# Kernel tuning notes

Measured on AMD Instinct MI355X. Metric: run time of the kernel, lower is better.

Reference implementation:

```python
import jax, jax.numpy as jnp
import numpy as np

NB_HEAD = 16
SIZE_PER_HEAD = 64
D_MODEL = NB_HEAD * SIZE_PER_HEAD  # 1024
B, L = 2, 2048
NEG_BIG = 1e12


def setup_inputs() -> dict:
    key = jax.random.key(0)
    ks = jax.random.split(key, 8)
    return {
        "Q_seq": jax.random.normal(ks[0], (B, L, D_MODEL), dtype=jnp.float32),
        "K_seq": jax.random.normal(ks[1], (B, L, D_MODEL), dtype=jnp.float32),
        "V_seq": jax.random.normal(ks[2], (B, L, D_MODEL), dtype=jnp.float32),
        "q_len": jax.random.randint(ks[3], (B, 1), 1, L, dtype=jnp.int32),
        "v_len": jax.random.randint(ks[4], (B, 1), 1, L, dtype=jnp.int32),
        "WQ": jax.random.normal(ks[5], (D_MODEL, D_MODEL), dtype=jnp.float32) * 0.02,
        "WK": jax.random.normal(ks[6], (D_MODEL, D_MODEL), dtype=jnp.float32) * 0.02,
        "WV": jax.random.normal(ks[7], (D_MODEL, D_MODEL), dtype=jnp.float32) * 0.02,
    }


def _len_mask(lens, length, dtype):
    # Keras code: mask = 1 - cumsum(one_hot(len, L)) -> 1 for pos < len, 0 otherwise
    return (jnp.arange(length)[None, :] < lens).astype(dtype)  # [B, L]


def reference(Q_seq, K_seq, V_seq, q_len, v_len, WQ, WK, WV):
    Bq, Lq, _ = Q_seq.shape
    Lk = K_seq.shape[1]
    # QKV projections, split heads: [B, H, L, D]
    q = (Q_seq @ WQ).reshape(Bq, Lq, NB_HEAD, SIZE_PER_HEAD).transpose(0, 2, 1, 3)
    k = (K_seq @ WK).reshape(Bq, Lk, NB_HEAD, SIZE_PER_HEAD).transpose(0, 2, 1, 3)
    v = (V_seq @ WV).reshape(Bq, Lk, NB_HEAD, SIZE_PER_HEAD).transpose(0, 2, 1, 3)
    # scaled dot-product scores [B, H, Lq, Lk]
    scores = jnp.einsum("bhqd,bhkd->bhqk", q, k) / np.float32(SIZE_PER_HEAD ** 0.5)
    # additive key-length mask (V_len), matching Mask(..., 'add')
    kmask = _len_mask(v_len, Lk, scores.dtype)  # [B, Lk]
    scores = scores - (1.0 - kmask)[:, None, None, :] * np.float32(NEG_BIG)
    A = jax.nn.softmax(scores, axis=-1)
    # attention output, merge heads: [B, Lq, H*D]
    O = jnp.einsum("bhqk,bhkd->bqhd", A, v).reshape(Bq, Lq, D_MODEL)
    # multiplicative query-length mask (Q_len), matching Mask(..., 'mul')
    qmask = _len_mask(q_len, Lq, O.dtype)  # [B, Lq]
    return O * qmask[:, :, None]
```

## Files before the change

kernel.cpp:

```cpp
#include <hip/hip_runtime.h>
#include <cstddef>

#define NB_HEAD 16
#define HEAD_DIM 64
#define D_MODEL 1024
#define BATCH 2
#define SEQ 2048
#define MROWS (BATCH * SEQ)
#define NSPLIT 2

typedef __bf16 bf16x8 __attribute__((ext_vector_type(8)));
typedef __bf16 bf16x4 __attribute__((ext_vector_type(4)));
typedef float  f32x4  __attribute__((ext_vector_type(4)));

#define XEL ((size_t)MROWS * D_MODEL)
#define WEL ((size_t)D_MODEL * D_MODEL)

#define QSCALE 0.18033688011112042f

static __device__ __forceinline__ size_t xchunk(int row, int k) {
    return ((size_t)(row >> 4) * 32 + (k >> 5)) * 512 + ((k >> 3) & 3) * 128 + (row & 15) * 8 + (k & 7);
}
static __device__ __forceinline__ size_t qkbase(int bh, int row16, int dc) {
    return ((size_t)(bh * 128 + row16) * 2 + dc) * 512;
}
static __device__ __forceinline__ size_t qkelem(int bh, int row, int d) {
    return qkbase(bh, row >> 4, d >> 5) + ((d >> 3) & 3) * 128 + (row & 15) * 8 + (d & 7);
}
static __device__ __forceinline__ size_t vbase(int bh, int d16, int kc) {
    return ((size_t)(bh * 4 + d16) * 64 + kc) * 512;
}
static __device__ __forceinline__ size_t velem(int bh, int d, int key) {
    return vbase(bh, d >> 4, key >> 5) + ((key >> 3) & 3) * 128 + (d & 15) * 8 + (key & 7);
}

static __device__ __forceinline__ void split_bf16(float x, __bf16& h, __bf16& l) {
    h = (__bf16)x;
    l = (__bf16)(x - (float)h);
}

static __device__ __forceinline__ void gload_lds16(const __bf16* g, __bf16* l) {
    __builtin_amdgcn_global_load_lds((const __attribute__((address_space(1))) void*)g,
                                     (__attribute__((address_space(3))) void*)l,
                                     16, 0, 0);
}

__global__ __launch_bounds__(256) void conv_wt_kernel(
    const float* __restrict__ W0, const float* __restrict__ W1,
    const float* __restrict__ W2,
    __bf16* __restrict__ hi, __bf16* __restrict__ lo)
{
    __shared__ float tile[64][65];
    const int t  = threadIdx.x;
    const int k0 = blockIdx.x * 64;
    const int n0 = blockIdx.y * 64;
    const int z  = blockIdx.z;
    const float* W = (z == 0) ? W0 : ((z == 1) ? W1 : W2);
    __bf16* hz = hi + (size_t)z * WEL;
    __bf16* lz = lo + (size_t)z * WEL;

    #pragma unroll
    for (int p = 0; p < 4; ++p) {
        const int e = (p * 256 + t) * 4;
        const int r = e >> 6, c = e & 63;
        const float4 v = *(const float4*)(W + (size_t)(k0 + r) * D_MODEL + n0 + c);
        tile[r][c] = v.x; tile[r][c + 1] = v.y; tile[r][c + 2] = v.z; tile[r][c + 3] = v.w;
    }
    __syncthreads();
    #pragma unroll
    for (int p = 0; p < 4; ++p) {
        const int e = (p * 256 + t) * 4;
        const int n = e >> 6, kc = e & 63;
        __bf16 h[4], l[4];
        #pragma unroll
        for (int u = 0; u < 4; ++u) split_bf16(tile[kc + u][n], h[u], l[u]);
        const size_t a = xchunk(n0 + n, k0 + kc);
        *(bf16x4*)(hz + a) = (bf16x4){h[0], h[1], h[2], h[3]};
        *(bf16x4*)(lz + a) = (bf16x4){l[0], l[1], l[2], l[3]};
    }
}

__global__ __launch_bounds__(256) void conv_x_kernel(
    const float* __restrict__ X0, const float* __restrict__ X1,
    const float* __restrict__ X2,
    const int* __restrict__ q_len, const int* __restrict__ v_len,
    __bf16* __restrict__ xhi, __bf16* __restrict__ xlo)
{
    const int z = blockIdx.y;
    const size_t e = ((size_t)blockIdx.x * 256 + threadIdx.x) * 8;
    const int l = (int)(e >> 10), k = (int)(e & 1023);
    const int bb = l >> 11, lb = l & (SEQ - 1);
    const int len = (z == 0) ? q_len[bb] : v_len[bb];
    if (lb >= ((len + 127) & ~127)) return;

    const float* X = (z == 0) ? X0 : ((z == 1) ? X1 : X2);
    const float4 v0 = *(const float4*)(X + e);
    const float4 v1 = *(const float4*)(X + e + 4);
    const float xs[8] = {v0.x, v0.y, v0.z, v0.w, v1.x, v1.y, v1.z, v1.w};
    bf16x8 h8, l8;
    #pragma unroll
    for (int u = 0; u < 8; ++u) { __bf16 h_, l_; split_bf16(xs[u], h_, l_); h8[u] = h_; l8[u] = l_; }
    const size_t a = z * XEL + xchunk(l, k);
    *(bf16x8*)(xhi + a) = h8;
    *(bf16x8*)(xlo + a) = l8;
}

__global__ __launch_bounds__(256, 3) void proj_mfma_kernel(
    const __bf16* __restrict__ Xhi, const __bf16* __restrict__ Xlo,
    const __bf16* __restrict__ Wchi, const __bf16* __restrict__ Wclo,
    const int* __restrict__ q_len, const int* __restrict__ v_len,
    __bf16* __restrict__ qch, __bf16* __restrict__ qcl,
    __bf16* __restrict__ kch, __bf16* __restrict__ kcl,
    __bf16* __restrict__ vch, __bf16* __restrict__ vcl)
{
    __shared__ __align__(16) __bf16 lds[2][24][512];

    const int t    = threadIdx.x;
    const int wave = t >> 6, lane = t & 63;
    const int li   = lane & 15, grp = lane >> 4;
    const int wm   = wave >> 1, wn = wave & 1;
    const int m0   = blockIdx.x * 128;
    const int n0   = blockIdx.y * 64;
    const int z    = blockIdx.z;
    const int bb   = m0 >> 11;
    const int l0   = m0 & (SEQ - 1);
    const int need = (z == 0) ? q_len[bb] : v_len[bb];
    if (l0 >= need) return;

    const __bf16* Xh = Xhi + z * XEL;
    const __bf16* Xl = Xlo + z * XEL;
    const __bf16* Wh = Wchi + z * WEL;
    const __bf16* Wl = Wclo + z * WEL;

    const __bf16* gs[6];
    #pragma unroll
    for (int u = 0; u < 6; ++u) {
        const int c = u * 4 + wave;
        const __bf16* src;
        int idx;
        if (c < 8)       { src = Xh; idx = (m0 >> 4) + c; }
        else if (c < 16) { src = Xl; idx = (m0 >> 4) + (c - 8); }
        else if (c < 20) { src = Wh; idx = (n0 >> 4) + (c - 16); }
        else             { src = Wl; idx = (n0 >> 4) + (c - 20); }
        gs[u] = src + (size_t)idx * 32 * 512 + (size_t)lane * 8;
    }

    auto STAGE = [&](int buf, int kc) {
        #pragma unroll
        for (int u = 0; u < 6; ++u)
            gload_lds16(gs[u] + (size_t)kc * 512, &lds[buf][u * 4 + wave][0]);
    };

    f32x4 acc[4][2] = {};

    STAGE(0, 0);
    __syncthreads();

    #pragma unroll 2
    for (int kc = 0; kc < 32; ++kc) {
        const int cur = kc & 1;
        if (kc < 31) STAGE(cur ^ 1, kc + 1);

        bf16x8 ah[4], al4[4], bh2[2], bl2[2];
        #pragma unroll
        for (int i = 0; i < 4; ++i) {
            ah[i]  = *(const bf16x8*)&lds[cur][(wm << 2) + i][lane * 8];
            al4[i] = *(const bf16x8*)&lds[cur][8 + (wm << 2) + i][lane * 8];
        }
        #pragma unroll
        for (int j = 0; j < 2; ++j) {
            bh2[j] = *(const bf16x8*)&lds[cur][16 + (wn << 1) + j][lane * 8];
            bl2[j] = *(const bf16x8*)&lds[cur][20 + (wn << 1) + j][lane * 8];
        }
        #pragma unroll
        for (int j = 0; j < 2; ++j) {
            #pragma unroll
            for (int i = 0; i < 4; ++i) {
                acc[i][j] = __builtin_amdgcn_mfma_f32_16x16x32_bf16(ah[i],  bh2[j], acc[i][j], 0, 0, 0);
                acc[i][j] = __builtin_amdgcn_mfma_f32_16x16x32_bf16(ah[i],  bl2[j], acc[i][j], 0, 0, 0);
                acc[i][j] = __builtin_amdgcn_mfma_f32_16x16x32_bf16(al4[i], bh2[j], acc[i][j], 0, 0, 0);
            }
        }
        __syncthreads();
    }

    #pragma unroll
    for (int j = 0; j < 2; ++j) {
        const int cg = n0 + wn * 32 + j * 16 + li;
        const int hd = cg >> 6, d = cg & 63;
        const int bhI = bb * NB_HEAD + hd;
        #pragma unroll
        for (int i = 0; i < 4; ++i) {
            #pragma unroll
            for (int r = 0; r < 4; ++r) {
                const int rg = m0 + wm * 64 + i * 16 + grp * 4 + r;
                const int lg = rg & (SEQ - 1);
                __bf16 h_, l_;
                if (z == 0) {
                    split_bf16(acc[i][j][r] * QSCALE, h_, l_);
                    const size_t a = qkelem(bhI, lg, d);
                    qch[a] = h_; qcl[a] = l_;
                } else if (z == 1) {
                    split_bf16(acc[i][j][r], h_, l_);
                    const size_t a = qkelem(bhI, lg, d);
                    kch[a] = h_; kcl[a] = l_;
                } else {
                    split_bf16(acc[i][j][r], h_, l_);
                    const size_t a = velem(bhI, d, lg);
                    vch[a] = h_; vcl[a] = l_;
                }
            }
        }
    }
}

__global__ __launch_bounds__(256, 2) void attn_mfma_kernel(
    const __bf16* __restrict__ qch, const __bf16* __restrict__ qcl,
    const __bf16* __restrict__ kch, const __bf16* __restrict__ kcl,
    const __bf16* __restrict__ vch, const __bf16* __restrict__ vcl,
    const int* __restrict__ q_len, const int* __restrict__ v_len,
    float* __restrict__ Opart, float* __restrict__ Mbuf, float* __restrict__ Lbuf)
{
    __shared__ __align__(16) __bf16 Ps[128][72];

    const int t = threadIdx.x;
    const int wq = t >> 6, lane = t & 63;
    const int grp = lane >> 4, li = lane & 15;
    const int hh = blockIdx.x;
    const int split = blockIdx.y & (NSPLIT - 1);
    const int q0 = (blockIdx.y >> 1) * 128;
    const int b  = blockIdx.z;
    const int qlen = q_len[b], vlen = v_len[b];
    const int bh = b * NB_HEAD + hh;
    const int qbase = q0 + wq * 32;

    if (qbase >= qlen) return;

    bf16x8 onesv;
    #pragma unroll
    for (int u = 0; u < 8; ++u) onesv[u] = (__bf16)1.0f;

    bf16x8 qh[2][2], ql[2][2];
    #pragma unroll
    for (int s = 0; s < 2; ++s)
        #pragma unroll
        for (int ks = 0; ks < 2; ++ks) {
            const size_t a = qkbase(bh, (qbase >> 4) + s, ks) + lane * 8;
            qh[s][ks] = *(const bf16x8*)(qch + a);
            ql[s][ks] = *(const bf16x8*)(qcl + a);
        }

    f32x4 O[2][4] = {};
    float m_s[2][4], l_s[2][4];
    #pragma unroll
    for (int s = 0; s < 2; ++s)
        #pragma unroll
        for (int r = 0; r < 4; ++r) { m_s[s][r] = -1e30f; l_s[s][r] = 0.f; }

    const int nktT = (vlen + 63) >> 6;
    const int half = (nktT + NSPLIT - 1) / NSPLIT;
    const int tBeg = split * half;
    const int tEnd = (nktT < tBeg + half) ? nktT : (tBeg + half);

    for (int tt = tBeg; tt < tEnd; ++tt) {
        const int k0 = tt * 64;
        const bool full = (k0 + 64 <= vlen);

        f32x4 sacc[2][4] = {};
        #pragma unroll
        for (int ks = 0; ks < 2; ++ks) {
            bf16x8 kh_[4], kl_[4];
            #pragma unroll
            for (int j = 0; j < 4; ++j) {
                const size_t a = qkbase(bh, (k0 >> 4) + j, ks) + lane * 8;
                kh_[j] = *(const bf16x8*)(kch + a);
                kl_[j] = *(const bf16x8*)(kcl + a);
            }
            #pragma unroll
            for (int j = 0; j < 4; ++j)
                #pragma unroll
                for (int s = 0; s < 2; ++s) {
                    sacc[s][j] = __builtin_amdgcn_mfma_f32_16x16x32_bf16(qh[s][ks], kh_[j], sacc[s][j], 0, 0, 0);
                    sacc[s][j] = __builtin_amdgcn_mfma_f32_16x16x32_bf16(qh[s][ks], kl_[j], sacc[s][j], 0, 0, 0);
                    sacc[s][j] = __builtin_amdgcn_mfma_f32_16x16x32_bf16(ql[s][ks], kh_[j], sacc[s][j], 0, 0, 0);
                }
        }

        bf16x8 vh_[2][4], vl_[2][4];
        #pragma unroll
        for (int ks = 0; ks < 2; ++ks)
            #pragma unroll
            for (int j = 0; j < 4; ++j) {
                const size_t a = vbase(bh, j, (k0 >> 5) + ks) + lane * 8;
                vh_[ks][j] = *(const bf16x8*)(vch + a);
                vl_[ks][j] = *(const bf16x8*)(vcl + a);
            }

        float mxs[2][4];
        int defer = 1;
        #pragma unroll
        for (int s = 0; s < 2; ++s) {
            float mx[4] = {-1e30f, -1e30f, -1e30f, -1e30f};
            if (full) {
                #pragma unroll
                for (int j = 0; j < 4; ++j)
                    #pragma unroll
                    for (int r = 0; r < 4; ++r) mx[r] = fmaxf(mx[r], sacc[s][j][r]);
            } else {
                #pragma unroll
                for (int j = 0; j < 4; ++j) {
                    const int key = k0 + j * 16 + li;
                    #pragma unroll
                    for (int r = 0; r < 4; ++r) {
                        float v = sacc[s][j][r];
                        if (key >= vlen) v = -1e30f;
                        sacc[s][j][r] = v;
                        mx[r] = fmaxf(mx[r], v);
                    }
                }
            }
            #pragma unroll
            for (int r = 0; r < 4; ++r) {
                mx[r] = fmaxf(mx[r], __shfl_xor(mx[r], 1));
                mx[r] = fmaxf(mx[r], __shfl_xor(mx[r], 2));
                mx[r] = fmaxf(mx[r], __shfl_xor(mx[r], 4));
                mx[r] = fmaxf(mx[r], __shfl_xor(mx[r], 8));
                mxs[s][r] = mx[r];
                defer &= (mx[r] - m_s[s][r] <= 8.f) ? 1 : 0;
            }
        }

        if (!__all(defer)) {
            #pragma unroll
            for (int s = 0; s < 2; ++s) {
                float al[4];
                #pragma unroll
                for (int r = 0; r < 4; ++r) {
                    const float mn = fmaxf(m_s[s][r], mxs[s][r]);
                    al[r] = exp2f(m_s[s][r] - mn);
                    m_s[s][r] = mn;
                    l_s[s][r] *= al[r];
                }
                #pragma unroll
                for (int j = 0; j < 4; ++j)
                    #pragma unroll
                    for (int r = 0; r < 4; ++r) O[s][j][r] *= al[r];
            }
        }

        #pragma unroll
        for (int s = 0; s < 2; ++s)
            #pragma unroll
            for (int j = 0; j < 4; ++j)
                #pragma unroll
                for (int r = 0; r < 4; ++r) {
                    const float p = exp2f(sacc[s][j][r] - m_s[s][r]);
                    Ps[wq * 32 + s * 16 + grp * 4 + r][j * 16 + li] = (__bf16)p;
                }
        asm volatile("s_waitcnt lgkmcnt(0)" ::: "memory");

        bf16x8 pa[2][2];
        #pragma unroll
        for (int s = 0; s < 2; ++s)
            #pragma unroll
            for (int ks = 0; ks < 2; ++ks)
                pa[s][ks] = *(const bf16x8*)&Ps[wq * 32 + s * 16 + li][ks * 32 + grp * 8];

        #pragma unroll
        for (int s = 0; s < 2; ++s) {
            f32x4 lsum = {};
            lsum = __builtin_amdgcn_mfma_f32_16x16x32_bf16(pa[s][0], onesv, lsum, 0, 0, 0);
            lsum = __builtin_amdgcn_mfma_f32_16x16x32_bf16(pa[s][1], onesv, lsum, 0, 0, 0);
            #pragma unroll
            for (int r = 0; r < 4; ++r) l_s[s][r] += lsum[r];
        }

        #pragma unroll
        for (int ks = 0; ks < 2; ++ks)
            #pragma unroll
            for (int j = 0; j < 4; ++j)
                #pragma unroll
                for (int s = 0; s < 2; ++s) {
                    O[s][j] = __builtin_amdgcn_mfma_f32_16x16x32_bf16(pa[s][ks], vh_[ks][j], O[s][j], 0, 0, 0);
                    O[s][j] = __builtin_amdgcn_mfma_f32_16x16x32_bf16(pa[s][ks], vl_[ks][j], O[s][j], 0, 0, 0);
                }
    }

    const size_t osplit = (size_t)split * MROWS * D_MODEL;
    #pragma unroll
    for (int s = 0; s < 2; ++s)
        #pragma unroll
        for (int r = 0; r < 4; ++r) {
            const int q = qbase + s * 16 + grp * 4 + r;
            if (q < qlen) {
                #pragma unroll
                for (int j = 0; j < 4; ++j)
                    Opart[osplit + ((size_t)b * SEQ + q) * D_MODEL + hh * HEAD_DIM + j * 16 + li] = O[s][j][r];
                if (li == 0) {
                    const size_t mi = (((size_t)split * BATCH + b) * NB_HEAD + hh) * SEQ + q;
                    Mbuf[mi] = m_s[s][r];
                    Lbuf[mi] = l_s[s][r];
                }
            }
        }
}

__global__ __launch_bounds__(256) void attn_merge_kernel(
    const float* __restrict__ Opart, const float* __restrict__ Mbuf,
    const float* __restrict__ Lbuf, const int* __restrict__ q_len,
    float* __restrict__ out)
{
    const int row = blockIdx.x;
    const int b = row >> 11, q = row & (SEQ - 1);
    const int col = threadIdx.x * 4;
    const int hh = col >> 6;
    const size_t oidx = (size_t)row * D_MODEL + col;

    float4 o = make_float4(0.f, 0.f, 0.f, 0.f);
    if (q < q_len[b]) {
        const size_t mlsz = (size_t)BATCH * NB_HEAD * SEQ;
        const size_t mi = ((size_t)b * NB_HEAD + hh) * SEQ + q;
        const float m0 = Mbuf[mi], m1 = Mbuf[mlsz + mi];
        const float l0 = Lbuf[mi], l1 = Lbuf[mlsz + mi];
        const float M  = fmaxf(m0, m1);
        const float w0 = exp2f(m0 - M), w1 = exp2f(m1 - M);
        const float inv = 1.f / (l0 * w0 + l1 * w1);
        const float4 a = *(const float4*)(Opart + oidx);
        const float4 c = *(const float4*)(Opart + (size_t)MROWS * D_MODEL + oidx);
        o.x = (a.x * w0 + c.x * w1) * inv;
        o.y = (a.y * w0 + c.y * w1) * inv;
        o.z = (a.z * w0 + c.z * w1) * inv;
        o.w = (a.w * w0 + c.w * w1) * inv;
    }
    *(float4*)(out + oidx) = o;
}

extern "C" void kernel_launch(void* const* d_in, const int* in_sizes, int n_in,
                              void* d_out, int out_size, void* d_ws, size_t ws_size,
                              hipStream_t stream)
{
    (void)in_sizes; (void)n_in; (void)out_size; (void)ws_size;
    const float* Q_seq = (const float*)d_in[0];
    const float* K_seq = (const float*)d_in[1];
    const float* V_seq = (const float*)d_in[2];
    const int*   q_len = (const int*)d_in[3];
    const int*   v_len = (const int*)d_in[4];
    const float* WQ    = (const float*)d_in[5];
    const float* WK    = (const float*)d_in[6];
    const float* WV    = (const float*)d_in[7];
    float* out = (float*)d_out;

    __bf16* wchi = (__bf16*)d_ws;
    __bf16* wclo = wchi + 3 * WEL;
    __bf16* xhi_ = wclo + 3 * WEL;
    __bf16* xlo_ = xhi_ + 3 * XEL;
    __bf16* qch_ = xlo_ + 3 * XEL;
    __bf16* qcl_ = qch_ + XEL;
    __bf16* kch_ = qcl_ + XEL;
    __bf16* kcl_ = kch_ + XEL;
    __bf16* vch_ = kcl_ + XEL;
    __bf16* vcl_ = vch_ + XEL;

    float* Opart = (float*)xhi_;
    float* Mbuf  = (float*)wchi;
    float* Lbuf  = Mbuf + (size_t)NSPLIT * BATCH * NB_HEAD * SEQ;

    dim3 blk(256);

    dim3 cg(D_MODEL / 64, D_MODEL / 64, 3);
    conv_wt_kernel<<<cg, blk, 0, stream>>>(WQ, WK, WV, wchi, wclo);

    dim3 xg((unsigned)(XEL / 2048), 3);
    conv_x_kernel<<<xg, blk, 0, stream>>>(Q_seq, K_seq, V_seq, q_len, v_len, xhi_, xlo_);

    dim3 pg(MROWS / 128, D_MODEL / 64, 3);
    proj_mfma_kernel<<<pg, blk, 0, stream>>>(xhi_, xlo_, wchi, wclo, q_len, v_len,
                                             qch_, qcl_, kch_, kcl_, vch_, vcl_);

    dim3 ag(NB_HEAD, (SEQ / 128) * NSPLIT, BATCH);
    attn_mfma_kernel<<<ag, blk, 0, stream>>>(qch_, qcl_, kch_, kcl_, vch_, vcl_,
                                             q_len, v_len, Opart, Mbuf, Lbuf);

    attn_merge_kernel<<<dim3(MROWS), blk, 0, stream>>>(Opart, Mbuf, Lbuf, q_len, out);
}
```

Baseline: 272.5 us.

## Transpose QK^T MFMA so softmax row stats are per-lane, add setprio

```diff
diff --git a/kernel.cpp b/kernel.cpp
--- a/kernel.cpp
+++ b/kernel.cpp
@@ -11,6 +11,7 @@
 
 typedef __bf16 bf16x8 __attribute__((ext_vector_type(8)));
 typedef __bf16 bf16x4 __attribute__((ext_vector_type(4)));
+typedef __bf16 bf16x2 __attribute__((ext_vector_type(2)));
 typedef float  f32x4  __attribute__((ext_vector_type(4)));
 
 #define XEL ((size_t)MROWS * D_MODEL)
@@ -251,11 +252,12 @@
         }
 
     f32x4 O[2][4] = {};
-    float m_s[2][4], l_s[2][4];
+    float m_s[2] = {-1e30f, -1e30f};
+    float l_s[2][4];
     #pragma unroll
     for (int s = 0; s < 2; ++s)
         #pragma unroll
-        for (int r = 0; r < 4; ++r) { m_s[s][r] = -1e30f; l_s[s][r] = 0.f; }
+        for (int r = 0; r < 4; ++r) l_s[s][r] = 0.f;
 
     const int nktT = (vlen + 63) >> 6;
     const int half = (nktT + NSPLIT - 1) / NSPLIT;
@@ -276,14 +278,16 @@
                 kh_[j] = *(const bf16x8*)(kch + a);
                 kl_[j] = *(const bf16x8*)(kcl + a);
             }
+            __builtin_amdgcn_s_setprio(1);
             #pragma unroll
             for (int j = 0; j < 4; ++j)
                 #pragma unroll
                 for (int s = 0; s < 2; ++s) {
-                    sacc[s][j] = __builtin_amdgcn_mfma_f32_16x16x32_bf16(qh[s][ks], kh_[j], sacc[s][j], 0, 0, 0);
-                    sacc[s][j] = __builtin_amdgcn_mfma_f32_16x16x32_bf16(qh[s][ks], kl_[j], sacc[s][j], 0, 0, 0);
-                    sacc[s][j] = __builtin_amdgcn_mfma_f32_16x16x32_bf16(ql[s][ks], kh_[j], sacc[s][j], 0, 0, 0);
-                }
+                    sacc[s][j] = __builtin_amdgcn_mfma_f32_16x16x32_bf16(kh_[j], qh[s][ks], sacc[s][j], 0, 0, 0);
+                    sacc[s][j] = __builtin_amdgcn_mfma_f32_16x16x32_bf16(kl_[j], qh[s][ks], sacc[s][j], 0, 0, 0);
+                    sacc[s][j] = __builtin_amdgcn_mfma_f32_16x16x32_bf16(kh_[j], ql[s][ks], sacc[s][j], 0, 0, 0);
+                }
+            __builtin_amdgcn_s_setprio(0);
         }
 
         bf16x8 vh_[2][4], vl_[2][4];
@@ -296,67 +300,61 @@
                 vl_[ks][j] = *(const bf16x8*)(vcl + a);
             }
 
-        float mxs[2][4];
+        float mx[2];
         int defer = 1;
         #pragma unroll
         for (int s = 0; s < 2; ++s) {
-            float mx[4] = {-1e30f, -1e30f, -1e30f, -1e30f};
-            if (full) {
-                #pragma unroll
-                for (int j = 0; j < 4; ++j)
+            if (!full) {
+                #pragma unroll
+                for (int j = 0; j < 4; ++j) {
+                    const int keyb = k0 + j * 16 + grp * 4;
                     #pragma unroll
-                    for (int r = 0; r < 4; ++r) mx[r] = fmaxf(mx[r], sacc[s][j][r]);
-            } else {
-                #pragma unroll
-                for (int j = 0; j < 4; ++j) {
-                    const int key = k0 + j * 16 + li;
+                    for (int r = 0; r < 4; ++r)
+                        if (keyb + r >= vlen) sacc[s][j][r] = -1e30f;
+                }
+            }
+            float m0_ = -1e30f;
+            #pragma unroll
+            for (int j = 0; j < 4; ++j)
+                #pragma unroll
+                for (int r = 0; r < 4; ++r) m0_ = fmaxf(m0_, sacc[s][j][r]);
+            m0_ = fmaxf(m0_, __shfl_xor(m0_, 16));
+            m0_ = fmaxf(m0_, __shfl_xor(m0_, 32));
+            mx[s] = m0_;
+            defer &= (m0_ - m_s[s] <= 8.f) ? 1 : 0;
+        }
+
+        if (!__all(defer)) {
+            #pragma unroll
+            for (int s = 0; s < 2; ++s) {
+                const float mn = fmaxf(m_s[s], mx[s]);
+                const float alq = exp2f(m_s[s] - mn);
+                m_s[s] = mn;
+                #pragma unroll
+                for (int r = 0; r < 4; ++r) {
+                    const float alr = __shfl(alq, grp * 4 + r);
+                    l_s[s][r] *= alr;
                     #pragma unroll
-                    for (int r = 0; r < 4; ++r) {
-                        float v = sacc[s][j][r];
-                        if (key >= vlen) v = -1e30f;
-                        sacc[s][j][r] = v;
-                        mx[r] = fmaxf(mx[r], v);
-                    }
-                }
-            }
-            #pragma unroll
-            for (int r = 0; r < 4; ++r) {
-                mx[r] = fmaxf(mx[r], __shfl_xor(mx[r], 1));
-                mx[r] = fmaxf(mx[r], __shfl_xor(mx[r], 2));
-                mx[r] = fmaxf(mx[r], __shfl_xor(mx[r], 4));
-                mx[r] = fmaxf(mx[r], __shfl_xor(mx[r], 8));
-                mxs[s][r] = mx[r];
-                defer &= (mx[r] - m_s[s][r] <= 8.f) ? 1 : 0;
-            }
-        }
-
-        if (!__all(defer)) {
-            #pragma unroll
-            for (int s = 0; s < 2; ++s) {
-                float al[4];
-                #pragma unroll
-                for (int r = 0; r < 4; ++r) {
-                    const float mn = fmaxf(m_s[s][r], mxs[s][r]);
-                    al[r] = exp2f(m_s[s][r] - mn);
-                    m_s[s][r] = mn;
-                    l_s[s][r] *= al[r];
-                }
-                #pragma unroll
-                for (int j = 0; j < 4; ++j)
-                    #pragma unroll
-                    for (int r = 0; r < 4; ++r) O[s][j][r] *= al[r];
-            }
-        }
-
-        #pragma unroll
-        for (int s = 0; s < 2; ++s)
-            #pragma unroll
-            for (int j = 0; j < 4; ++j)
-                #pragma unroll
-                for (int r = 0; r < 4; ++r) {
-                    const float p = exp2f(sacc[s][j][r] - m_s[s][r]);
-                    Ps[wq * 32 + s * 16 + grp * 4 + r][j * 16 + li] = (__bf16)p;
-                }
+                    for (int j = 0; j < 4; ++j) O[s][j][r] *= alr;
+                }
+            }
+        }
+
+        #pragma unroll
+        for (int s = 0; s < 2; ++s) {
+            const int row = wq * 32 + s * 16 + li;
+            #pragma unroll
+            for (int j = 0; j < 4; ++j) {
+                const int col = j * 16 + grp * 4;
+                bf16x2 w01, w23;
+                w01[0] = (__bf16)exp2f(sacc[s][j][0] - m_s[s]);
+                w01[1] = (__bf16)exp2f(sacc[s][j][1] - m_s[s]);
+                w23[0] = (__bf16)exp2f(sacc[s][j][2] - m_s[s]);
+                w23[1] = (__bf16)exp2f(sacc[s][j][3] - m_s[s]);
+                *(bf16x2*)&Ps[row][col]     = w01;
+                *(bf16x2*)&Ps[row][col + 2] = w23;
+            }
+        }
         asm volatile("s_waitcnt lgkmcnt(0)" ::: "memory");
 
         bf16x8 pa[2][2];
@@ -366,6 +364,7 @@
             for (int ks = 0; ks < 2; ++ks)
                 pa[s][ks] = *(const bf16x8*)&Ps[wq * 32 + s * 16 + li][ks * 32 + grp * 8];
 
+        __builtin_amdgcn_s_setprio(1);
         #pragma unroll
         for (int s = 0; s < 2; ++s) {
             f32x4 lsum = {};
@@ -384,6 +383,7 @@
                     O[s][j] = __builtin_amdgcn_mfma_f32_16x16x32_bf16(pa[s][ks], vh_[ks][j], O[s][j], 0, 0, 0);
                     O[s][j] = __builtin_amdgcn_mfma_f32_16x16x32_bf16(pa[s][ks], vl_[ks][j], O[s][j], 0, 0, 0);
                 }
+        __builtin_amdgcn_s_setprio(0);
     }
 
     const size_t osplit = (size_t)split * MROWS * D_MODEL;
@@ -398,11 +398,18 @@
                     Opart[osplit + ((size_t)b * SEQ + q) * D_MODEL + hh * HEAD_DIM + j * 16 + li] = O[s][j][r];
                 if (li == 0) {
                     const size_t mi = (((size_t)split * BATCH + b) * NB_HEAD + hh) * SEQ + q;
-                    Mbuf[mi] = m_s[s][r];
                     Lbuf[mi] = l_s[s][r];
                 }
             }
         }
+    #pragma unroll
+    for (int s = 0; s < 2; ++s) {
+        const int q = qbase + s * 16 + li;
+        if (grp == 0 && q < qlen) {
+            const size_t mi = (((size_t)split * BATCH + b) * NB_HEAD + hh) * SEQ + q;
+            Mbuf[mi] = m_s[s];
+        }
+    }
 }
 
 __global__ __launch_bounds__(256) void attn_merge_kernel(
```

After: 258.4 us. 5.2% less time.
